# Kernel optimization log

Measured on AMD Instinct MI355X. Metric: run time of the kernel, lower is better.

Reference implementation:

```python
import jax, jax.numpy as jnp
import numpy as np

B, C, H, W = 64, 512, 32, 32
N, K = 4, 1024          # num_codebooks, num_embeddings
D = C // N              # dims per codebook = 128


def setup_inputs() -> dict:
    key = jax.random.key(0)
    k1, k2 = jax.random.split(key)
    x = jax.random.normal(k1, (B, C, H, W), dtype=jnp.float32)
    embed = jax.random.normal(k2, (N, D, K), dtype=jnp.float32)  # codebooks
    return {"x": x, "embed": embed}


def reference(x, embed):
    """QLayer.up with downsample==1: identity encoder -> multi-codebook VQ.
    Returns (z_q [B,C,H,W], diff scalar, argmin [B,N,H,W], ppl scalar)."""
    P = B * H * W
    # channels-last, split channels into N codebooks of D dims each
    z = jnp.transpose(x, (0, 2, 3, 1)).reshape(P, N, D)          # [P,N,D]
    # squared L2 distance: ||z||^2 - 2 z.e + ||e||^2   -> [P,N,K]
    dist = (jnp.sum(z * z, axis=-1, keepdims=True)
            - 2.0 * jnp.einsum('pnd,ndk->pnk', z, embed)
            + jnp.sum(embed * embed, axis=1)[None])
    idx = jnp.argmin(dist, axis=-1)                              # [P,N] int
    # gather nearest codewords: embed_t [N,K,D]
    embed_t = jnp.transpose(embed, (0, 2, 1))
    q = embed_t[jnp.arange(N)[None, :], idx]                     # [P,N,D]
    q = q.reshape(B, H, W, C)
    z_bhwc = jnp.transpose(x, (0, 2, 3, 1))
    # commitment term and straight-through estimator
    diff = jnp.mean(jnp.square(jax.lax.stop_gradient(q) - z_bhwc))
    z_q = z_bhwc + jax.lax.stop_gradient(q - z_bhwc)
    z_q = jnp.transpose(z_q, (0, 3, 1, 2))                       # [B,C,H,W]
    # perplexity of codebook usage (mean over codebooks)
    counts = jnp.zeros((N, K), jnp.float32).at[
        jnp.broadcast_to(jnp.arange(N)[None, :], idx.shape), idx].add(1.0)
    probs = counts / P
    ppl = jnp.mean(jnp.exp(-jnp.sum(probs * jnp.log(probs + 1e-10), axis=-1)))
    argmin = jnp.transpose(idx.reshape(B, H, W, N), (0, 3, 1, 2))  # [B,N,H,W]
    return z_q, diff, argmin, ppl
```

## Files before the change

kernel.cpp:

```cpp
#include <hip/hip_runtime.h>
#include <math.h>

#define BB  64
#define CC  512
#define NN  4
#define KK  1024
#define DD  128
#define HW  1024
#define PP  65536

#define OFF_DIFF 33554432UL
#define OFF_ARG  33554433UL
#define OFF_PPL  33816577UL

#define WS_HIST   0
#define WS_DSUM   16384
#define WS_WLCNT  16392
#define WS_ENORM  16416
#define WS_EBF    32800
#define WS_EMBT   (32800 + 128*8192)
#define WS_WL     (WS_EMBT + NN*KK*DD*4)

#define DELTA 0.0625f

typedef _Float16 half8 __attribute__((ext_vector_type(8)));
typedef float f32x4 __attribute__((ext_vector_type(4)));

#define MFMA16(a, b, c) __builtin_amdgcn_mfma_f32_16x16x32_f16(a, b, c, 0, 0, 0)

__device__ __forceinline__ int swz(int row, int dbyte) {
    return (row * 256 + dbyte) ^ ((row & 15) << 4);
}
__device__ __forceinline__ void gl2lds16(const void* g, void* l) {
    __builtin_amdgcn_global_load_lds(
        (const __attribute__((address_space(1))) unsigned int*)g,
        (__attribute__((address_space(3))) unsigned int*)l, 16, 0, 0);
}

__global__ __launch_bounds__(256) void vq_prep(const float* __restrict__ embed,
                                               char* __restrict__ ebf,
                                               float* __restrict__ embt,
                                               float* __restrict__ enorm,
                                               unsigned* __restrict__ hist,
                                               double* __restrict__ dsum,
                                               unsigned* __restrict__ wlcnt) {
    __shared__ float sred[16][16];
    const int e = blockIdx.x;
    const int n = e >> 6, kt16 = e & 63, k0 = kt16 * 16;
    const int t = threadIdx.x, kr = t & 15, dc = t >> 4;
    if (t < 16) hist[e * 16 + t] = 0u;
    if (e == 0 && t == 0) { *dsum = 0.0; *wlcnt = 0u; }

    const float* src = embed + ((size_t)n * DD + dc * 8) * KK + k0 + kr;
    char* tile = ebf + ((size_t)(n * 32 + (kt16 >> 1))) * 8192;
    const int row = (kt16 & 1) * 16 + kr;
    float fv[8];
    #pragma unroll
    for (int r = 0; r < 8; ++r) fv[r] = src[(size_t)r * KK];
    float s = 0.f;
    half8 vh;
    #pragma unroll
    for (int r = 0; r < 8; ++r) {
        vh[r] = (_Float16)fv[r];
        s = fmaf(fv[r], fv[r], s);
    }
    *(half8*)(tile + swz(row, dc * 16)) = vh;
    {
        float* drow = embt + ((size_t)n * KK + k0 + kr) * DD + dc * 8;
        *(float4*)(drow)     = make_float4(fv[0], fv[1], fv[2], fv[3]);
        *(float4*)(drow + 4) = make_float4(fv[4], fv[5], fv[6], fv[7]);
    }
    sred[dc][kr] = s;
    __syncthreads();
    if (t < 16) {
        float a = 0.f;
        #pragma unroll
        for (int d2 = 0; d2 < 16; ++d2) a += sred[d2][t];
        enorm[n * KK + k0 + t] = -0.5f * a;
    }
}

#define TOP2(C0, C1, MF, KP)                                                  \
    _Pragma("unroll")                                                         \
    for (int i_ = 0; i_ < 4; ++i_) {                                          \
        float v_ = C0[i_] + C1[i_];                                           \
        int r_ = (MF) * 4 + i_;                                               \
        float mn_ = fminf(pb1[r_], v_);                                       \
        pb2[r_] = fmaxf(pb2[r_], mn_);                                        \
        pk1[r_] = (v_ > pb1[r_]) ? (KP) : pk1[r_];                            \
        pb1[r_] = fmaxf(pb1[r_], v_);                                         \
    }

#define VSTEP(ACW, ACR, KTL, KPREV)                                           \
  {                                                                           \
    if (gW < 128) {                                                           \
        const char* s_ = ebf + (size_t)gW * 8192 + t * 16;                    \
        char* d_ = ebase + (bufW << 13) + t * 16;                             \
        gl2lds16(s_, d_);                                                     \
        gl2lds16(s_ + 4096, d_ + 4096);                                       \
    }                                                                         \
    ++gW; bufW = (bufW == 5) ? 0 : bufW + 1;                                  \
    const int rb_ = bufR << 13;                                               \
    bufR = (bufR == 5) ? 0 : bufR + 1;                                        \
    half8 bh0 = *(const half8*)(ebase + rb_ + bo0);                           \
    half8 bh1 = *(const half8*)(ebase + rb_ + bo1);                           \
    half8 bh2 = *(const half8*)(ebase + rb_ + bo2);                           \
    half8 bh3 = *(const half8*)(ebase + rb_ + bo3);                           \
    float e2a = enls[((KTL) << 5) + koff];                                    \
    f32x4 e2v = {e2a, e2a, e2a, e2a};                                         \
    __builtin_amdgcn_s_setprio(1);                                            \
    ACW##00 = MFMA16(af[0][0], bh0, e2v);                                     \
    ACW##00 = MFMA16(af[0][1], bh1, ACW##00);                                 \
    ACW##01 = MFMA16(af[0][2], bh2, zz4);                                     \
    ACW##01 = MFMA16(af[0][3], bh3, ACW##01);                                 \
    ACW##10 = MFMA16(af[1][0], bh0, e2v);                                     \
    ACW##10 = MFMA16(af[1][1], bh1, ACW##10);                                 \
    ACW##11 = MFMA16(af[1][2], bh2, zz4);                                     \
    ACW##11 = MFMA16(af[1][3], bh3, ACW##11);                                 \
    __builtin_amdgcn_s_setprio(0);                                            \
    TOP2(ACR##00, ACR##01, 0, KPREV);                                         \
    TOP2(ACR##10, ACR##11, 1, KPREV);                                         \
  }

__global__ __launch_bounds__(256, 2) void vq_main(const float* __restrict__ x,
                                                  const char* __restrict__ ebf,
                                                  const float* __restrict__ embt,
                                                  const float* __restrict__ enormg,
                                                  float* __restrict__ out,
                                                  unsigned* __restrict__ hist,
                                                  double* __restrict__ dsum,
                                                  unsigned* __restrict__ wlcnt,
                                                  int2* __restrict__ wl, int wlcap) {
    __shared__ __attribute__((aligned(16))) _Float16 zs[64 * 128];
    __shared__ __attribute__((aligned(16))) char ebuf[6][8192];
    __shared__ __attribute__((aligned(16))) float enls[KK];
    __shared__ int   idx_s[64];
    __shared__ float red_b1[2][64], red_b2[2][64];
    __shared__ int   red_k1[2][64];
    __shared__ float wsum[4];

    const int t   = threadIdx.x;
    const int blk = blockIdx.x;
    const int b   = blk >> 4;
    const int hw0 = (blk & 15) << 6;
    const int w  = t >> 6, l = t & 63;
    const int pq = w >> 1;
    const int ks = w & 1;
    const int tk = l & 15, lg = l >> 4;
    const int koff = ks * 16 + tk;

    char* ebase = (char*)&ebuf[0][0];
    const int bo0 = swz(koff, (0 * 32 + lg * 8) * 2);
    const int bo1 = swz(koff, (1 * 32 + lg * 8) * 2);
    const int bo2 = swz(koff, (2 * 32 + lg * 8) * 2);
    const int bo3 = swz(koff, (3 * 32 + lg * 8) * 2);

    const f32x4 zz4 = {0.f, 0.f, 0.f, 0.f};
    const f32x4 m1e30 = {-1e30f, -1e30f, -1e30f, -1e30f};

    int bufR = 0, bufW = 4, gW = 4;
    float znacc = 0.f, sumb1 = 0.f;

    for (int n = 0; n < NN; ++n) {
        __syncthreads();
        gl2lds16((const char*)(enormg + n * KK) + t * 16, (char*)enls + t * 16);
        if (n == 0) {
            #pragma unroll
            for (int j = 0; j < 4; ++j) {
                const char* s_ = ebf + (size_t)j * 8192 + t * 16;
                char* d_ = ebase + j * 8192 + t * 16;
                gl2lds16(s_, d_);
                gl2lds16(s_ + 4096, d_ + 4096);
            }
        }
        {
            const int p = t & 63, dchunk = t >> 6;
            const float* xp = x + ((size_t)b * CC + n * DD + dchunk * 32) * HW + hw0 + p;
            float fv[32];
            #pragma unroll
            for (int r = 0; r < 32; ++r) fv[r] = xp[(size_t)r * HW];
            #pragma unroll
            for (int j = 0; j < 4; ++j) {
                half8 vh;
                #pragma unroll
                for (int r = 0; r < 8; ++r) {
                    float f = fv[j * 8 + r];
                    vh[r] = (_Float16)f;
                    znacc = fmaf(f, f, znacc);
                }
                *(half8*)((char*)zs + swz(p, (dchunk * 32 + j * 8) * 2)) = vh;
            }
        }
        __syncthreads();

        half8 af[2][4];
        #pragma unroll
        for (int mf = 0; mf < 2; ++mf)
            #pragma unroll
            for (int ds = 0; ds < 4; ++ds)
                af[mf][ds] = *(const half8*)((const char*)zs +
                               swz(pq * 32 + mf * 16 + tk, (ds * 32 + lg * 8) * 2));

        float pb1[8], pb2[8]; int pk1[8];
        #pragma unroll
        for (int r = 0; r < 8; ++r) { pb1[r] = -INFINITY; pb2[r] = -INFINITY; pk1[r] = 0; }

        f32x4 accA00, accA01, accA10, accA11;
        f32x4 accB00 = m1e30, accB01 = m1e30, accB10 = m1e30, accB11 = m1e30;

        #pragma unroll 1
        for (int wnd = 0; wnd < 16; ++wnd) {
            if (n == NN - 1 && wnd == 15)
                asm volatile("s_waitcnt vmcnt(0)" ::: "memory");
            else
                asm volatile("s_waitcnt vmcnt(4)" ::: "memory");
            __builtin_amdgcn_s_barrier();
            __builtin_amdgcn_sched_barrier(0);
            const int ka = wnd * 2;
            VSTEP(accA, accB, ka,     ((ka - 1) << 5) + koff)
            VSTEP(accB, accA, ka + 1, (ka << 5) + koff)
        }
        TOP2(accB00, accB01, 0, (31 << 5) + koff);
        TOP2(accB10, accB11, 1, (31 << 5) + koff);

        #pragma unroll
        for (int off = 1; off < 16; off <<= 1) {
            #pragma unroll
            for (int r = 0; r < 8; ++r) {
                float ob1 = __shfl_xor(pb1[r], off);
                float ob2 = __shfl_xor(pb2[r], off);
                int   ok1 = __shfl_xor(pk1[r], off);
                float nb2 = fmaxf(pb2[r], ob2);
                if (ob1 > pb1[r] || (ob1 == pb1[r] && ok1 < pk1[r])) {
                    pb2[r] = fmaxf(nb2, pb1[r]); pb1[r] = ob1; pk1[r] = ok1;
                } else {
                    pb2[r] = fmaxf(nb2, ob1);
                }
            }
        }
        if (tk == 0) {
            #pragma unroll
            for (int mf = 0; mf < 2; ++mf)
                #pragma unroll
                for (int i = 0; i < 4; ++i) {
                    int p = pq * 32 + mf * 16 + lg * 4 + i, r = mf * 4 + i;
                    red_b1[ks][p] = pb1[r]; red_b2[ks][p] = pb2[r]; red_k1[ks][p] = pk1[r];
                }
        }
        __syncthreads();
        if (t < 64) {
            int p = t;
            float m1 = red_b1[0][p], m2 = red_b2[0][p]; int mk = red_k1[0][p];
            {
                float ob1 = red_b1[1][p], ob2 = red_b2[1][p]; int ok = red_k1[1][p];
                float nb2 = fmaxf(m2, ob2);
                if (ob1 > m1 || (ob1 == m1 && ok < mk)) { m2 = fmaxf(nb2, m1); m1 = ob1; mk = ok; }
                else                                    { m2 = fmaxf(nb2, ob1); }
            }
            idx_s[p] = mk;
            atomicAdd(&hist[n * KK + mk], 1u);
            sumb1 += m1;
            if ((m1 - m2) < DELTA * 0.5f) {
                unsigned pos = atomicAdd(wlcnt, 1u);
                if ((int)pos < wlcap) wl[pos] = make_int2(b * HW + hw0 + p, n);
            }
            out[OFF_ARG + (size_t)b * (NN * HW) + (size_t)n * HW + hw0 + p] = (float)mk;
        }
        __syncthreads();

        {
            const int pp = (t & 31) * 2, cc8 = t >> 5;
            const int ka = idx_s[pp], kb = idx_s[pp + 1];
            const float4* ra = (const float4*)(embt + ((size_t)n * KK + ka) * DD + cc8 * 16);
            const float4* rb = (const float4*)(embt + ((size_t)n * KK + kb) * DD + cc8 * 16);
            float4 qa0 = ra[0], qa1 = ra[1], qa2 = ra[2], qa3 = ra[3];
            float4 qb0 = rb[0], qb1 = rb[1], qb2 = rb[2], qb3 = rb[3];
            float qa[16] = {qa0.x,qa0.y,qa0.z,qa0.w, qa1.x,qa1.y,qa1.z,qa1.w,
                            qa2.x,qa2.y,qa2.z,qa2.w, qa3.x,qa3.y,qa3.z,qa3.w};
            float qb[16] = {qb0.x,qb0.y,qb0.z,qb0.w, qb1.x,qb1.y,qb1.z,qb1.w,
                            qb2.x,qb2.y,qb2.z,qb2.w, qb3.x,qb3.y,qb3.z,qb3.w};
            #pragma unroll
            for (int j = 0; j < 16; ++j) {
                *(float2*)&out[((size_t)b * CC + n * DD + cc8 * 16 + j) * HW + hw0 + pp]
                    = make_float2(qa[j], qb[j]);
            }
        }
    }

    {
        float tot = znacc - 2.f * sumb1;
        #pragma unroll
        for (int off = 32; off > 0; off >>= 1) tot += __shfl_down(tot, off);
        if (l == 0) wsum[w] = tot;
        __syncthreads();
        if (t == 0) {
            double sd = 0.0;
            #pragma unroll
            for (int ww = 0; ww < 4; ++ww) sd += (double)wsum[ww];
            atomicAdd(dsum, sd);
        }
    }
}

#define ACCQ(U, V, J)                                                         \
  { double a0_ = (double)(V).x, a1_ = (double)(V).y,                          \
           a2_ = (double)(V).z, a3_ = (double)(V).w;                          \
    U = fma(a0_, zd2[(J)*4+0] - a0_, U);                                      \
    U = fma(a1_, zd2[(J)*4+1] - a1_, U);                                      \
    U = fma(a2_, zd2[(J)*4+2] - a2_, U);                                      \
    U = fma(a3_, zd2[(J)*4+3] - a3_, U); }

__global__ __launch_bounds__(256) void vq_refine(const float* __restrict__ x,
                                                 const float* __restrict__ embt,
                                                 float* __restrict__ out,
                                                 unsigned* __restrict__ hist,
                                                 const unsigned* __restrict__ wlcnt,
                                                 const int2* __restrict__ wl, int wlcap) {
    __shared__ float  zrow[DD];
    __shared__ double wbest[4];
    __shared__ int    wbestk[4];
    __shared__ int    flip_s;
    const int t = threadIdx.x;
    const int w = t >> 6, l = t & 63;
    const int rlane = l >> 3;
    const int dseg  = l & 7;

    unsigned wc = *wlcnt;
    int nitems = (int)(wc < (unsigned)wlcap ? wc : (unsigned)wlcap);

    for (int it = blockIdx.x; it < nitems; it += gridDim.x) {
        __syncthreads();
        int2 item = wl[it];
        int p = item.x, n = item.y;
        int b = p >> 10, hw = p & 1023;

        if (t < DD) zrow[t] = x[((size_t)b * CC + n * DD + t) * HW + hw];
        __syncthreads();

        double zd2[16];
        #pragma unroll
        for (int i = 0; i < 16; ++i) zd2[i] = 2.0 * (double)zrow[dseg * 16 + i];

        const float* en = embt + (size_t)n * KK * DD;
        double best = -INFINITY; int bestk = 0;
        const int rbase = w * 256;

        #pragma unroll 1
        for (int g0 = 0; g0 < 32; g0 += 2) {
            const int rowA = rbase + g0 * 8 + rlane;
            const int rowB = rowA + 8;
            const float4* erA = (const float4*)(en + (size_t)rowA * DD + dseg * 16);
            const float4* erB = (const float4*)(en + (size_t)rowB * DD + dseg * 16);
            float4 va0 = erA[0], va1 = erA[1], va2 = erA[2], va3 = erA[3];
            float4 vb0 = erB[0], vb1 = erB[1], vb2 = erB[2], vb3 = erB[3];
            double uA = 0.0, uB = 0.0;
            ACCQ(uA, va0, 0) ACCQ(uA, va1, 1) ACCQ(uA, va2, 2) ACCQ(uA, va3, 3)
            ACCQ(uB, vb0, 0) ACCQ(uB, vb1, 1) ACCQ(uB, vb2, 2) ACCQ(uB, vb3, 3)
            uA += __shfl_xor(uA, 1); uB += __shfl_xor(uB, 1);
            uA += __shfl_xor(uA, 2); uB += __shfl_xor(uB, 2);
            uA += __shfl_xor(uA, 4); uB += __shfl_xor(uB, 4);
            if (uA > best) { best = uA; bestk = rowA; }
            if (uB > best) { best = uB; bestk = rowB; }
        }
        #pragma unroll
        for (int mask = 8; mask <= 32; mask <<= 1) {
            double ob = __shfl_xor(best, mask);
            int    ok = __shfl_xor(bestk, mask);
            if (ob > best || (ob == best && ok < bestk)) { best = ob; bestk = ok; }
        }
        if (l == 0) { wbest[w] = best; wbestk[w] = bestk; }
        __syncthreads();
        if (t == 0) {
            double m = wbest[0]; int mk = wbestk[0];
            #pragma unroll
            for (int ww = 1; ww < 4; ++ww)
                if (wbest[ww] > m) { m = wbest[ww]; mk = wbestk[ww]; }
            size_t slot = OFF_ARG + (size_t)b * (NN * HW) + (size_t)n * HW + hw;
            int oldk = (int)out[slot];
            flip_s = -1;
            if (mk != oldk) {
                out[slot] = (float)mk;
                atomicSub(&hist[n * KK + oldk], 1u);
                atomicAdd(&hist[n * KK + mk], 1u);
                flip_s = mk;
            }
        }
        __syncthreads();
        int fk = flip_s;
        if (fk >= 0 && t < DD)
            out[((size_t)b * CC + n * DD + t) * HW + hw] = en[(size_t)fk * DD + t];
    }
}

__global__ __launch_bounds__(256) void vq_final(const unsigned* __restrict__ hist,
                                                const double* __restrict__ dsum,
                                                float* __restrict__ out) {
    __shared__ double red[256];
    __shared__ double hn[NN];
    const int t = threadIdx.x;
    for (int n = 0; n < NN; ++n) {
        double acc = 0.0;
        for (int k = t; k < KK; k += 256) {
            double pr = (double)hist[n * KK + k] / (double)PP;
            acc += pr * log(pr + 1e-10);
        }
        red[t] = acc;
        __syncthreads();
        for (int off = 128; off > 0; off >>= 1) {
            if (t < off) red[t] += red[t + off];
            __syncthreads();
        }
        if (t == 0) hn[n] = red[0];
        __syncthreads();
    }
    if (t == 0) {
        double ppl = 0.0;
        for (int n = 0; n < NN; ++n) ppl += exp(-hn[n]);
        out[OFF_PPL]  = (float)(ppl * 0.25);
        out[OFF_DIFF] = (float)(*dsum / (double)((size_t)BB * CC * HW));
    }
}

extern "C" void kernel_launch(void* const* d_in, const int* in_sizes, int n_in,
                              void* d_out, int out_size, void* d_ws, size_t ws_size,
                              hipStream_t stream) {
    const float* x     = (const float*)d_in[0];
    const float* embed = (const float*)d_in[1];
    float* out = (float*)d_out;
    char*  ws  = (char*)d_ws;

    unsigned* hist   = (unsigned*)(ws + WS_HIST);
    double*   dsum   = (double*)  (ws + WS_DSUM);
    unsigned* wlcnt  = (unsigned*)(ws + WS_WLCNT);
    float*    enorm  = (float*)   (ws + WS_ENORM);
    char*     ebf    = ws + WS_EBF;
    float*    embt   = (float*)   (ws + WS_EMBT);
    int2*     wl     = (int2*)    (ws + WS_WL);

    long long cap = ((long long)ws_size - WS_WL) / (long long)sizeof(int2);
    int wlcap = cap < 0 ? 0 : (cap > 65536 ? 65536 : (int)cap);

    vq_prep  <<<256,  256, 0, stream>>>(embed, ebf, embt, enorm, hist, dsum, wlcnt);
    vq_main  <<<1024, 256, 0, stream>>>(x, ebf, embt, enorm, out, hist, dsum, wlcnt, wl, wlcap);
    vq_refine<<<2048, 256, 0, stream>>>(x, embt, out, hist, wlcnt, wl, wlcap);
    vq_final <<<1,    256, 0, stream>>>(hist, dsum, out);
}
```

Baseline: 321.7 us.

## Cut LDS and registers to fit three blocks per CU

Shrinks the codebook LDS ring from six to four 8KB buffers, with a prefetch distance of two tiles. The small reduction arrays are aliased onto the z tile, and the launch bound is raised to three blocks per CU. The split MFMA accumulators are merged into one chain per fragment, which saves registers and one add in the top-2 update. The cost is a full vmcnt(0) wait every window, which removes most of the prefetch overlap and adds a serial MFMA dependency chain, in return for higher occupancy.

```diff
diff --git a/kernel.cpp b/kernel.cpp
--- a/kernel.cpp
+++ b/kernel.cpp
@@ -80,10 +80,10 @@
     }
 }
 
-#define TOP2(C0, C1, MF, KP)                                                  \
+#define TOP2(C, MF, KP)                                                       \
     _Pragma("unroll")                                                         \
     for (int i_ = 0; i_ < 4; ++i_) {                                          \
-        float v_ = C0[i_] + C1[i_];                                           \
+        float v_ = C[i_];                                                     \
         int r_ = (MF) * 4 + i_;                                               \
         float mn_ = fminf(pb1[r_], v_);                                       \
         pb2[r_] = fmaxf(pb2[r_], mn_);                                        \
@@ -95,13 +95,12 @@
   {                                                                           \
     if (gW < 128) {                                                           \
         const char* s_ = ebf + (size_t)gW * 8192 + t * 16;                    \
-        char* d_ = ebase + (bufW << 13) + t * 16;                             \
+        char* d_ = ebase + ((gW & 3) << 13) + t * 16;                         \
         gl2lds16(s_, d_);                                                     \
         gl2lds16(s_ + 4096, d_ + 4096);                                       \
     }                                                                         \
-    ++gW; bufW = (bufW == 5) ? 0 : bufW + 1;                                  \
-    const int rb_ = bufR << 13;                                               \
-    bufR = (bufR == 5) ? 0 : bufR + 1;                                        \
+    ++gW;                                                                     \
+    const int rb_ = (((n << 5) + (KTL)) & 3) << 13;                           \
     half8 bh0 = *(const half8*)(ebase + rb_ + bo0);                           \
     half8 bh1 = *(const half8*)(ebase + rb_ + bo1);                           \
     half8 bh2 = *(const half8*)(ebase + rb_ + bo2);                           \
@@ -109,20 +108,20 @@
     float e2a = enls[((KTL) << 5) + koff];                                    \
     f32x4 e2v = {e2a, e2a, e2a, e2a};                                         \
     __builtin_amdgcn_s_setprio(1);                                            \
-    ACW##00 = MFMA16(af[0][0], bh0, e2v);                                     \
-    ACW##00 = MFMA16(af[0][1], bh1, ACW##00);                                 \
-    ACW##01 = MFMA16(af[0][2], bh2, zz4);                                     \
-    ACW##01 = MFMA16(af[0][3], bh3, ACW##01);                                 \
-    ACW##10 = MFMA16(af[1][0], bh0, e2v);                                     \
-    ACW##10 = MFMA16(af[1][1], bh1, ACW##10);                                 \
-    ACW##11 = MFMA16(af[1][2], bh2, zz4);                                     \
-    ACW##11 = MFMA16(af[1][3], bh3, ACW##11);                                 \
+    ACW##0 = MFMA16(af[0][0], bh0, e2v);                                      \
+    ACW##0 = MFMA16(af[0][1], bh1, ACW##0);                                   \
+    ACW##0 = MFMA16(af[0][2], bh2, ACW##0);                                   \
+    ACW##0 = MFMA16(af[0][3], bh3, ACW##0);                                   \
+    ACW##1 = MFMA16(af[1][0], bh0, e2v);                                      \
+    ACW##1 = MFMA16(af[1][1], bh1, ACW##1);                                   \
+    ACW##1 = MFMA16(af[1][2], bh2, ACW##1);                                   \
+    ACW##1 = MFMA16(af[1][3], bh3, ACW##1);                                   \
     __builtin_amdgcn_s_setprio(0);                                            \
-    TOP2(ACR##00, ACR##01, 0, KPREV);                                         \
-    TOP2(ACR##10, ACR##11, 1, KPREV);                                         \
+    TOP2(ACR##0, 0, KPREV);                                                   \
+    TOP2(ACR##1, 1, KPREV);                                                   \
   }
 
-__global__ __launch_bounds__(256, 2) void vq_main(const float* __restrict__ x,
+__global__ __launch_bounds__(256, 3) void vq_main(const float* __restrict__ x,
                                                   const char* __restrict__ ebf,
                                                   const float* __restrict__ embt,
                                                   const float* __restrict__ enormg,
@@ -132,12 +131,13 @@
                                                   unsigned* __restrict__ wlcnt,
                                                   int2* __restrict__ wl, int wlcap) {
     __shared__ __attribute__((aligned(16))) _Float16 zs[64 * 128];
-    __shared__ __attribute__((aligned(16))) char ebuf[6][8192];
+    __shared__ __attribute__((aligned(16))) char ebuf[4][8192];
     __shared__ __attribute__((aligned(16))) float enls[KK];
-    __shared__ int   idx_s[64];
-    __shared__ float red_b1[2][64], red_b2[2][64];
-    __shared__ int   red_k1[2][64];
-    __shared__ float wsum[4];
+    int*   idx_s  = (int*)zs;
+    float* red_b1 = (float*)((char*)zs + 256);
+    float* red_b2 = (float*)((char*)zs + 768);
+    int*   red_k1 = (int*)  ((char*)zs + 1280);
+    float* wsum   = (float*)((char*)zs + 1792);
 
     const int t   = threadIdx.x;
     const int blk = blockIdx.x;
@@ -155,10 +155,9 @@
     const int bo2 = swz(koff, (2 * 32 + lg * 8) * 2);
     const int bo3 = swz(koff, (3 * 32 + lg * 8) * 2);
 
-    const f32x4 zz4 = {0.f, 0.f, 0.f, 0.f};
     const f32x4 m1e30 = {-1e30f, -1e30f, -1e30f, -1e30f};
 
-    int bufR = 0, bufW = 4, gW = 4;
+    int gW = 2;
     float znacc = 0.f, sumb1 = 0.f;
 
     for (int n = 0; n < NN; ++n) {
@@ -166,7 +165,7 @@
         gl2lds16((const char*)(enormg + n * KK) + t * 16, (char*)enls + t * 16);
         if (n == 0) {
             #pragma unroll
-            for (int j = 0; j < 4; ++j) {
+            for (int j = 0; j < 2; ++j) {
                 const char* s_ = ebf + (size_t)j * 8192 + t * 16;
                 char* d_ = ebase + j * 8192 + t * 16;
                 gl2lds16(s_, d_);
@@ -205,23 +204,20 @@
         #pragma unroll
         for (int r = 0; r < 8; ++r) { pb1[r] = -INFINITY; pb2[r] = -INFINITY; pk1[r] = 0; }
 
-        f32x4 accA00, accA01, accA10, accA11;
-        f32x4 accB00 = m1e30, accB01 = m1e30, accB10 = m1e30, accB11 = m1e30;
+        f32x4 accA0, accA1;
+        f32x4 accB0 = m1e30, accB1 = m1e30;
 
         #pragma unroll 1
         for (int wnd = 0; wnd < 16; ++wnd) {
-            if (n == NN - 1 && wnd == 15)
-                asm volatile("s_waitcnt vmcnt(0)" ::: "memory");
-            else
-                asm volatile("s_waitcnt vmcnt(4)" ::: "memory");
+            asm volatile("s_waitcnt vmcnt(0)" ::: "memory");
             __builtin_amdgcn_s_barrier();
             __builtin_amdgcn_sched_barrier(0);
             const int ka = wnd * 2;
             VSTEP(accA, accB, ka,     ((ka - 1) << 5) + koff)
             VSTEP(accB, accA, ka + 1, (ka << 5) + koff)
         }
-        TOP2(accB00, accB01, 0, (31 << 5) + koff);
-        TOP2(accB10, accB11, 1, (31 << 5) + koff);
+        TOP2(accB0, 0, (31 << 5) + koff);
+        TOP2(accB1, 1, (31 << 5) + koff);
 
         #pragma unroll
         for (int off = 1; off < 16; off <<= 1) {
@@ -244,15 +240,17 @@
                 #pragma unroll
                 for (int i = 0; i < 4; ++i) {
                     int p = pq * 32 + mf * 16 + lg * 4 + i, r = mf * 4 + i;
-                    red_b1[ks][p] = pb1[r]; red_b2[ks][p] = pb2[r]; red_k1[ks][p] = pk1[r];
+                    red_b1[ks * 64 + p] = pb1[r];
+                    red_b2[ks * 64 + p] = pb2[r];
+                    red_k1[ks * 64 + p] = pk1[r];
                 }
         }
         __syncthreads();
         if (t < 64) {
             int p = t;
-            float m1 = red_b1[0][p], m2 = red_b2[0][p]; int mk = red_k1[0][p];
+            float m1 = red_b1[p], m2 = red_b2[p]; int mk = red_k1[p];
             {
-                float ob1 = red_b1[1][p], ob2 = red_b2[1][p]; int ok = red_k1[1][p];
+                float ob1 = red_b1[64 + p], ob2 = red_b2[64 + p]; int ok = red_k1[64 + p];
                 float nb2 = fmaxf(m2, ob2);
                 if (ob1 > m1 || (ob1 == m1 && ok < mk)) { m2 = fmaxf(nb2, m1); m1 = ob1; mk = ok; }
                 else                                    { m2 = fmaxf(nb2, ob1); }
@@ -270,9 +268,9 @@
 
         {
             const int pp = (t & 31) * 2, cc8 = t >> 5;
-            const int ka = idx_s[pp], kb = idx_s[pp + 1];
-            const float4* ra = (const float4*)(embt + ((size_t)n * KK + ka) * DD + cc8 * 16);
-            const float4* rb = (const float4*)(embt + ((size_t)n * KK + kb) * DD + cc8 * 16);
+            const int ka2 = idx_s[pp], kb2 = idx_s[pp + 1];
+            const float4* ra = (const float4*)(embt + ((size_t)n * KK + ka2) * DD + cc8 * 16);
+            const float4* rb = (const float4*)(embt + ((size_t)n * KK + kb2) * DD + cc8 * 16);
             float4 qa0 = ra[0], qa1 = ra[1], qa2 = ra[2], qa3 = ra[3];
             float4 qb0 = rb[0], qb1 = rb[1], qb2 = rb[2], qb3 = rb[3];
             float qa[16] = {qa0.x,qa0.y,qa0.z,qa0.w, qa1.x,qa1.y,qa1.z,qa1.w,
```

New measurement: 337.1 us. +4.8%, slower.
